# Kernel tuning notes

Hardware: AMD Instinct MI355X
Metric: run time of the kernel (lower is better)

The kernel has to match this reference:

```python
import jax, jax.numpy as jnp
import numpy as np
from jax import lax

BATCH, SEQ_LEN, HIDDEN, CLASSES = 512, 256, 1024, 128

def _xavier(key, shape):
    fan_out, fan_in = shape
    std = float(np.sqrt(2.0 / (fan_in + fan_out)))
    return jax.random.normal(key, shape, dtype=jnp.float32) * std

def setup_inputs() -> dict:
    key = jax.random.key(0)
    k_x, k_hx, k_hh, k_ph = jax.random.split(key, 4)
    return {
        "x": jax.random.normal(k_x, (BATCH, SEQ_LEN), dtype=jnp.float32),
        "W_hx": _xavier(k_hx, (HIDDEN, 1)),
        "W_hh": _xavier(k_hh, (HIDDEN, HIDDEN)),
        "b_h": jnp.zeros((HIDDEN,), dtype=jnp.float32),
        "W_ph": _xavier(k_ph, (CLASSES, HIDDEN)),
        "b_p": jnp.zeros((CLASSES,), dtype=jnp.float32),
    }

def reference(x, W_hx, W_hh, b_h, W_ph, b_p):
    # x: [B, T] (input_dim == 1 per timestep, as in the torch module)
    B = x.shape[0]
    H = W_hh.shape[0]
    h0 = jnp.zeros((B, H), dtype=x.dtype)

    def step(h, xt):
        # xt: [B]; xt[:, None] @ W_hx.T -> [B, H]
        h_new = jnp.tanh(xt[:, None] @ W_hx.T + h @ W_hh.T + b_h)
        return h_new, None

    h_last, _ = lax.scan(step, h0, x.T)  # scan over time: x.T is [T, B]
    # Output head applied to final hidden state (loop's last p in torch code)
    return h_last @ W_ph.T + b_p  # [B, num_classes]
```

## Files before the change

kernel.cpp:

```cpp
#include <hip/hip_runtime.h>
#include <stdint.h>


#define BATCH 512
#define SEQ   256
#define HID   1024
#define CLS   128

#define GB 16
#define GJ 16
#define BT 32
#define JT 64
#define KC 256
#define SSTR 260
#define HSTR 68
#define HS_OFF 16384
#define SMEM_BYTES (32768 + BT * HSTR * 2)
#define HBUF_HALVES (BATCH * HID)

typedef __attribute__((ext_vector_type(8))) short  bf16x8;
typedef __attribute__((ext_vector_type(4))) short  s16x4;
typedef __attribute__((ext_vector_type(4))) float  f32x4;
typedef __attribute__((ext_vector_type(4))) int    i32x4;
typedef __attribute__((ext_vector_type(2))) unsigned int u32x2;

__device__ __forceinline__ unsigned short f2bf(float f) {
  unsigned int u = __float_as_uint(f);
  u = (u + 0x7FFFu + ((u >> 16) & 1u)) >> 16;
  return (unsigned short)u;
}
__device__ __forceinline__ float b2f(short h) {
  return __uint_as_float(((unsigned int)(unsigned short)h) << 16);
}

__device__ __forceinline__ void store_flag(int* p, int v) {
  asm volatile("global_store_dword %0, %1, off sc0 sc1" :: "v"(p), "v"(v) : "memory");
}
__device__ __forceinline__ int load_flag(const int* p) {
  int v;
  asm volatile("global_load_dword %0, %1, off sc0 sc1\n\t"
               "s_waitcnt vmcnt(0)" : "=v"(v) : "v"(p) : "memory");
  return v;
}
__device__ __forceinline__ void store16(void* p, i32x4 v) {
  asm volatile("global_store_dwordx4 %0, %1, off sc0 sc1" :: "v"(p), "v"(v) : "memory");
}
__device__ __forceinline__ void waitcnt0() {
  asm volatile("s_waitcnt vmcnt(0)" ::: "memory");
}
__device__ __forceinline__ void barrier_lgkm() {
  asm volatile("s_waitcnt lgkmcnt(0)\n\ts_barrier" ::: "memory");
}
__device__ __forceinline__ void issue4(const void* p, i32x4& a, i32x4& b, i32x4& c, i32x4& d) {
  asm volatile(
    "global_load_dwordx4 %0, %4, off sc0 sc1\n\t"
    "global_load_dwordx4 %1, %4, off offset:128 sc0 sc1\n\t"
    "global_load_dwordx4 %2, %4, off offset:256 sc0 sc1\n\t"
    "global_load_dwordx4 %3, %4, off offset:384 sc0 sc1"
    : "=&v"(a), "=&v"(b), "=&v"(c), "=&v"(d)
    : "v"(p) : "memory");
}
__device__ __forceinline__ void issue4_64(const void* p, i32x4& a, i32x4& b, i32x4& c, i32x4& d) {
  asm volatile(
    "global_load_dwordx4 %0, %4, off sc0 sc1\n\t"
    "global_load_dwordx4 %1, %4, off offset:64 sc0 sc1\n\t"
    "global_load_dwordx4 %2, %4, off offset:128 sc0 sc1\n\t"
    "global_load_dwordx4 %3, %4, off offset:192 sc0 sc1"
    : "=&v"(a), "=&v"(b), "=&v"(c), "=&v"(d)
    : "v"(p) : "memory");
}

__device__ __forceinline__ void wr16(short* p, i32x4 v) {
  u32x2 lo, hi;
  lo.x = (unsigned)v.x; lo.y = (unsigned)v.y;
  hi.x = (unsigned)v.z; hi.y = (unsigned)v.w;
  *(u32x2*)p = lo;
  *(u32x2*)(p + 4) = hi;
}
__device__ __forceinline__ float tanh_fast(float z) {
  float e = __expf(2.f * z);
  return 1.f - 2.f / (e + 1.f);
}

#define MFMA(a, b, c) __builtin_amdgcn_mfma_f32_16x16x32_bf16((a), (b), (c), 0, 0, 0)

__global__ void __launch_bounds__(256, 1)
rnn_persistent(const float* __restrict__ x, const float* __restrict__ Whx,
               const float* __restrict__ Whh, const float* __restrict__ bh,
               const float* __restrict__ Wph, const float* __restrict__ bp,
               float* __restrict__ out, unsigned short* hbuf, int* flags)
{
  extern __shared__ short smem[];
  float* scr = (float*)smem;
  short* hS  = smem + HS_OFF;

  const int tid  = threadIdx.x;
  const int bg   = blockIdx.x & 15;
  const int jg   = blockIdx.x >> 4;
  const int lane = tid & 63;
  const int wv   = tid >> 6;
  const int l15  = lane & 15;
  const int quad = lane >> 4;

  bf16x8 barr[4][8];
#pragma unroll
  for (int ct = 0; ct < 4; ++ct) {
#pragma unroll
    for (int ks = 0; ks < 8; ++ks) {
      const float* wp = Whh + (jg * JT + ct * 16 + l15) * HID
                            + wv * 256 + ks * 32 + quad * 8;
      float4 fA = *(const float4*)(wp);
      float4 fB = *(const float4*)(wp + 4);
      union { bf16x8 v8; s16x4 h[2]; } u;
      u.h[0].x = (short)f2bf(fA.x); u.h[0].y = (short)f2bf(fA.y);
      u.h[0].z = (short)f2bf(fA.z); u.h[0].w = (short)f2bf(fA.w);
      u.h[1].x = (short)f2bf(fB.x); u.h[1].y = (short)f2bf(fB.y);
      u.h[1].z = (short)f2bf(fB.z); u.h[1].w = (short)f2bf(fB.w);
      barr[ct][ks] = u.v8;
    }
  }

  const int j = jg * JT + wv * 16 + l15;
  const float whx = Whx[j];
  const float bhv = bh[j];
  const int grow0 = bg * BT + quad * 4;

  const int sr  = tid >> 3;
  const int seg = tid & 7;

  int* myflags = flags + bg * 64;

  for (int t = 0; t < SEQ; ++t) {
    const unsigned short* hin = hbuf + ((t + 1) & 1) * HBUF_HALVES;
    unsigned short*      hout = hbuf + (t & 1) * HBUF_HALVES;

    f32x4 acc00 = {0,0,0,0}, acc01 = {0,0,0,0}, acc02 = {0,0,0,0}, acc03 = {0,0,0,0};
    f32x4 acc10 = {0,0,0,0}, acc11 = {0,0,0,0}, acc12 = {0,0,0,0}, acc13 = {0,0,0,0};

    float xv0[4], xv1[4];
    {
      const float* xp = x + grow0 * SEQ + t;
#pragma unroll
      for (int rg = 0; rg < 4; ++rg) {
        xv0[rg] = xp[rg * SEQ];
        xv1[rg] = xp[(16 + rg) * SEQ];
      }
    }

    if (t > 0) {
      if (lane < 4) {
        while (load_flag(myflags + wv * 4 + lane) < t) {
          asm volatile("s_sleep 1" ::: "memory");
        }
      }

      const short* pA0 = (const short*)hin + (bg * BT + l15) * HID
                         + wv * 256 + quad * 8;
      const short* pA1 = pA0 + 16 * HID;
      i32x4 A0, A1, A2, A3, A4, A5, A6, A7, A8, A9, A10, A11, A12, A13, A14, A15;
      issue4_64(pA0,        A0,  A1,  A2,  A3);
      issue4_64(pA0 + 128,  A4,  A5,  A6,  A7);
      issue4_64(pA1,        A8,  A9,  A10, A11);
      issue4_64(pA1 + 128,  A12, A13, A14, A15);

      asm volatile("s_waitcnt vmcnt(0)"
                   : "+v"(A0), "+v"(A1), "+v"(A2),  "+v"(A3),
                     "+v"(A4), "+v"(A5), "+v"(A6),  "+v"(A7),
                     "+v"(A8), "+v"(A9), "+v"(A10), "+v"(A11),
                     "+v"(A12), "+v"(A13), "+v"(A14), "+v"(A15)
                   :: "memory");
      __builtin_amdgcn_sched_barrier(0);

#define KSTEP(Ar0, Ar1, KS) { \
      bf16x8 _a0 = *(const bf16x8*)&(Ar0); \
      bf16x8 _a1 = *(const bf16x8*)&(Ar1); \
      acc00 = MFMA(_a0, barr[0][KS], acc00); acc10 = MFMA(_a1, barr[0][KS], acc10); \
      acc01 = MFMA(_a0, barr[1][KS], acc01); acc11 = MFMA(_a1, barr[1][KS], acc11); \
      acc02 = MFMA(_a0, barr[2][KS], acc02); acc12 = MFMA(_a1, barr[2][KS], acc12); \
      acc03 = MFMA(_a0, barr[3][KS], acc03); acc13 = MFMA(_a1, barr[3][KS], acc13); }
      KSTEP(A0, A8,  0) KSTEP(A1, A9,  1) KSTEP(A2, A10, 2) KSTEP(A3, A11, 3)
      KSTEP(A4, A12, 4) KSTEP(A5, A13, 5) KSTEP(A6, A14, 6) KSTEP(A7, A15, 7)
#undef KSTEP
    }

    barrier_lgkm();
#pragma unroll
    for (int ct = 0; ct < 4; ++ct) {
      f32x4 w0 = (ct == 0) ? acc00 : (ct == 1) ? acc01 : (ct == 2) ? acc02 : acc03;
      f32x4 w1 = (ct == 0) ? acc10 : (ct == 1) ? acc11 : (ct == 2) ? acc12 : acc13;
      *(f32x4*)(scr + (((ct * 2 + 0) * 4 + wv) * 64 + lane) * 4) = w0;
      *(f32x4*)(scr + (((ct * 2 + 1) * 4 + wv) * 64 + lane) * 4) = w1;
    }
    barrier_lgkm();
    {
      f32x4 f0 = {0,0,0,0}, f1 = {0,0,0,0};
#pragma unroll
      for (int w = 0; w < 4; ++w) {
        f0 += *(const f32x4*)(scr + (((wv * 2 + 0) * 4 + w) * 64 + lane) * 4);
        f1 += *(const f32x4*)(scr + (((wv * 2 + 1) * 4 + w) * 64 + lane) * 4);
      }
#pragma unroll
      for (int rg = 0; rg < 4; ++rg) {
        float z0 = f0[rg] + xv0[rg] * whx + bhv;
        hS[(quad * 4 + rg) * HSTR + wv * 16 + l15] = (short)f2bf(tanh_fast(z0));
        float z1 = f1[rg] + xv1[rg] * whx + bhv;
        hS[(16 + quad * 4 + rg) * HSTR + wv * 16 + l15] = (short)f2bf(tanh_fast(z1));
      }
    }
    barrier_lgkm();
    {
      const short* hsrc = hS + sr * HSTR + seg * 8;
      u32x2 lo = *(const u32x2*)(hsrc);
      u32x2 hi = *(const u32x2*)(hsrc + 4);
      i32x4 sv; sv.x = (int)lo.x; sv.y = (int)lo.y; sv.z = (int)hi.x; sv.w = (int)hi.y;
      unsigned short* dst = hout + (bg * BT + sr) * HID + jg * JT + seg * 8;
      store16(dst, sv);
    }
    waitcnt0();
    barrier_lgkm();
    if (tid == 0) store_flag(myflags + jg, t + 1);
  }

  if (tid < GJ) {
    while (load_flag(myflags + tid) < SEQ) {
      asm volatile("s_sleep 1" ::: "memory");
    }
  }
  __syncthreads();

  const unsigned short* hlast = hbuf + ((SEQ - 1) & 1) * HBUF_HALVES;
  short* sS = smem;
  const int cc = tid & 7;
  const int cg = jg * 8 + cc;
  const int hr = tid >> 3;
  float acc = 0.f;
  const char* lbase = (const char*)(hlast + (bg * BT + sr) * HID) + seg * 16;
  short* sdst = sS + sr * SSTR + seg * 8;
  for (int c = 0; c < 4; ++c) {
    __syncthreads();
    i32x4 p0, p1, p2, p3;
    issue4(lbase + c * 512, p0, p1, p2, p3);
    waitcnt0();
    wr16(sdst, p0); wr16(sdst + 64, p1); wr16(sdst + 128, p2); wr16(sdst + 192, p3);
    __syncthreads();
    const float* wp = Wph + cg * HID + c * KC;
    const short* hs = sS + hr * SSTR;
#pragma unroll 8
    for (int k4 = 0; k4 < 64; ++k4) {
      float4 w  = *(const float4*)(wp + k4 * 4);
      s16x4 hv  = *(const s16x4*)(hs + k4 * 4);
      acc += b2f(hv.x) * w.x + b2f(hv.y) * w.y + b2f(hv.z) * w.z + b2f(hv.w) * w.w;
    }
  }
  out[(bg * BT + hr) * CLS + cg] = acc + bp[cg];
}

extern "C" void kernel_launch(void* const* d_in, const int* in_sizes, int n_in,
                              void* d_out, int out_size, void* d_ws, size_t ws_size,
                              hipStream_t stream) {
  const float* x   = (const float*)d_in[0];
  const float* Whx = (const float*)d_in[1];
  const float* Whh = (const float*)d_in[2];
  const float* bh  = (const float*)d_in[3];
  const float* Wph = (const float*)d_in[4];
  const float* bp  = (const float*)d_in[5];
  float* out = (float*)d_out;

  unsigned short* hbuf = (unsigned short*)d_ws;
  int* flags = (int*)((char*)d_ws + (size_t)2 * HBUF_HALVES * 2);

  hipMemsetAsync(flags, 0, GB * 64 * sizeof(int), stream);

  hipFuncSetAttribute(reinterpret_cast<const void*>(rnn_persistent),
                      hipFuncAttributeMaxDynamicSharedMemorySize, SMEM_BYTES);

  rnn_persistent<<<dim3(GB * GJ), dim3(256), SMEM_BYTES, stream>>>(
      x, Whx, Whh, bh, Wph, bp, out, hbuf, flags);
}
```

Baseline: 1.156 ms.

## Repartition persistent RNN grid into 32 batch groups by 8 hidden groups

Reshapes the persistent grid from 16x16 tiles (32 batch rows x 64 hidden columns) to 32x8 tiles (16 batch rows x 128 hidden columns). Each block now keeps twice as many W_hh register fragments and loads half as much h per step. Each batch group waits on 8 producer flags instead of 16, and a block-wide sync is added after the flag poll. The output-head epilogue stages the whole final hidden row into shared memory at once instead of in four chunks. This cuts per-step cross-block synchronisation fan-in and h traffic, at the cost of higher register pressure, which could cause spills.

Measured after the change: 966.0 us, median of 2. 16.4% less time.

```diff
diff --git a/kernel.cpp b/kernel.cpp
--- a/kernel.cpp
+++ b/kernel.cpp
@@ -7,13 +7,11 @@
 #define HID   1024
 #define CLS   128
 
-#define GB 16
-#define GJ 16
-#define BT 32
-#define JT 64
-#define KC 256
-#define SSTR 260
-#define HSTR 68
+#define GB 32
+#define GJ 8
+#define BT 16
+#define JT 128
+#define HSTR 132
 #define HS_OFF 16384
 #define SMEM_BYTES (32768 + BT * HSTR * 2)
 #define HBUF_HALVES (BATCH * HID)
@@ -50,15 +48,6 @@
 }
 __device__ __forceinline__ void barrier_lgkm() {
   asm volatile("s_waitcnt lgkmcnt(0)\n\ts_barrier" ::: "memory");
-}
-__device__ __forceinline__ void issue4(const void* p, i32x4& a, i32x4& b, i32x4& c, i32x4& d) {
-  asm volatile(
-    "global_load_dwordx4 %0, %4, off sc0 sc1\n\t"
-    "global_load_dwordx4 %1, %4, off offset:128 sc0 sc1\n\t"
-    "global_load_dwordx4 %2, %4, off offset:256 sc0 sc1\n\t"
-    "global_load_dwordx4 %3, %4, off offset:384 sc0 sc1"
-    : "=&v"(a), "=&v"(b), "=&v"(c), "=&v"(d)
-    : "v"(p) : "memory");
 }
 __device__ __forceinline__ void issue4_64(const void* p, i32x4& a, i32x4& b, i32x4& c, i32x4& d) {
   asm volatile(
@@ -66,6 +55,15 @@
     "global_load_dwordx4 %1, %4, off offset:64 sc0 sc1\n\t"
     "global_load_dwordx4 %2, %4, off offset:128 sc0 sc1\n\t"
     "global_load_dwordx4 %3, %4, off offset:192 sc0 sc1"
+    : "=&v"(a), "=&v"(b), "=&v"(c), "=&v"(d)
+    : "v"(p) : "memory");
+}
+__device__ __forceinline__ void issue4_16(const void* p, i32x4& a, i32x4& b, i32x4& c, i32x4& d) {
+  asm volatile(
+    "global_load_dwordx4 %0, %4, off sc0 sc1\n\t"
+    "global_load_dwordx4 %1, %4, off offset:16 sc0 sc1\n\t"
+    "global_load_dwordx4 %2, %4, off offset:32 sc0 sc1\n\t"
+    "global_load_dwordx4 %3, %4, off offset:48 sc0 sc1"
     : "=&v"(a), "=&v"(b), "=&v"(c), "=&v"(d)
     : "v"(p) : "memory");
 }
@@ -95,16 +93,16 @@
   short* hS  = smem + HS_OFF;
 
   const int tid  = threadIdx.x;
-  const int bg   = blockIdx.x & 15;
-  const int jg   = blockIdx.x >> 4;
+  const int bg   = blockIdx.x & 31;
+  const int jg   = blockIdx.x >> 5;
   const int lane = tid & 63;
   const int wv   = tid >> 6;
   const int l15  = lane & 15;
   const int quad = lane >> 4;
 
-  bf16x8 barr[4][8];
-#pragma unroll
-  for (int ct = 0; ct < 4; ++ct) {
+  bf16x8 barr[8][8];
+#pragma unroll
+  for (int ct = 0; ct < 8; ++ct) {
 #pragma unroll
     for (int ks = 0; ks < 8; ++ks) {
       const float* wp = Whh + (jg * JT + ct * 16 + l15) * HID
@@ -120,13 +118,13 @@
     }
   }
 
-  const int j = jg * JT + wv * 16 + l15;
-  const float whx = Whx[j];
-  const float bhv = bh[j];
-  const int grow0 = bg * BT + quad * 4;
-
-  const int sr  = tid >> 3;
-  const int seg = tid & 7;
+  const int j0 = jg * JT + wv * 32 + l15;
+  const int j1 = j0 + 16;
+  const float whx0 = Whx[j0], whx1 = Whx[j1];
+  const float bhv0 = bh[j0],  bhv1 = bh[j1];
+
+  const int sr  = tid >> 4;
+  const int seg = tid & 15;
 
   int* myflags = flags + bg * 64;
 
@@ -134,77 +132,69 @@
     const unsigned short* hin = hbuf + ((t + 1) & 1) * HBUF_HALVES;
     unsigned short*      hout = hbuf + (t & 1) * HBUF_HALVES;
 
-    f32x4 acc00 = {0,0,0,0}, acc01 = {0,0,0,0}, acc02 = {0,0,0,0}, acc03 = {0,0,0,0};
-    f32x4 acc10 = {0,0,0,0}, acc11 = {0,0,0,0}, acc12 = {0,0,0,0}, acc13 = {0,0,0,0};
-
-    float xv0[4], xv1[4];
+    f32x4 acc0 = {0,0,0,0}, acc1 = {0,0,0,0}, acc2 = {0,0,0,0}, acc3 = {0,0,0,0};
+    f32x4 acc4 = {0,0,0,0}, acc5 = {0,0,0,0}, acc6 = {0,0,0,0}, acc7 = {0,0,0,0};
+
+    float xv[4];
     {
-      const float* xp = x + grow0 * SEQ + t;
-#pragma unroll
-      for (int rg = 0; rg < 4; ++rg) {
-        xv0[rg] = xp[rg * SEQ];
-        xv1[rg] = xp[(16 + rg) * SEQ];
-      }
+      const float* xp = x + (bg * BT + quad * 4) * SEQ + t;
+#pragma unroll
+      for (int rg = 0; rg < 4; ++rg) xv[rg] = xp[rg * SEQ];
     }
 
     if (t > 0) {
-      if (lane < 4) {
-        while (load_flag(myflags + wv * 4 + lane) < t) {
+      if (tid < GJ) {
+        while (load_flag(myflags + tid) < t) {
           asm volatile("s_sleep 1" ::: "memory");
         }
       }
-
-      const short* pA0 = (const short*)hin + (bg * BT + l15) * HID
-                         + wv * 256 + quad * 8;
-      const short* pA1 = pA0 + 16 * HID;
-      i32x4 A0, A1, A2, A3, A4, A5, A6, A7, A8, A9, A10, A11, A12, A13, A14, A15;
-      issue4_64(pA0,        A0,  A1,  A2,  A3);
-      issue4_64(pA0 + 128,  A4,  A5,  A6,  A7);
-      issue4_64(pA1,        A8,  A9,  A10, A11);
-      issue4_64(pA1 + 128,  A12, A13, A14, A15);
+      __syncthreads();
+
+      const short* pA = (const short*)hin + (bg * BT + l15) * HID
+                        + wv * 256 + quad * 8;
+      i32x4 A0, A1, A2, A3, A4, A5, A6, A7;
+      issue4_64(pA,       A0, A1, A2, A3);
+      issue4_64(pA + 128, A4, A5, A6, A7);
 
       asm volatile("s_waitcnt vmcnt(0)"
-                   : "+v"(A0), "+v"(A1), "+v"(A2),  "+v"(A3),
-                     "+v"(A4), "+v"(A5), "+v"(A6),  "+v"(A7),
-                     "+v"(A8), "+v"(A9), "+v"(A10), "+v"(A11),
-                     "+v"(A12), "+v"(A13), "+v"(A14), "+v"(A15)
+                   : "+v"(A0), "+v"(A1), "+v"(A2), "+v"(A3),
+                     "+v"(A4), "+v"(A5), "+v"(A6), "+v"(A7)
                    :: "memory");
       __builtin_amdgcn_sched_barrier(0);
 
-#define KSTEP(Ar0, Ar1, KS) { \
-      bf16x8 _a0 = *(const bf16x8*)&(Ar0); \
-      bf16x8 _a1 = *(const bf16x8*)&(Ar1); \
-      acc00 = MFMA(_a0, barr[0][KS], acc00); acc10 = MFMA(_a1, barr[0][KS], acc10); \
-      acc01 = MFMA(_a0, barr[1][KS], acc01); acc11 = MFMA(_a1, barr[1][KS], acc11); \
-      acc02 = MFMA(_a0, barr[2][KS], acc02); acc12 = MFMA(_a1, barr[2][KS], acc12); \
-      acc03 = MFMA(_a0, barr[3][KS], acc03); acc13 = MFMA(_a1, barr[3][KS], acc13); }
-      KSTEP(A0, A8,  0) KSTEP(A1, A9,  1) KSTEP(A2, A10, 2) KSTEP(A3, A11, 3)
-      KSTEP(A4, A12, 4) KSTEP(A5, A13, 5) KSTEP(A6, A14, 6) KSTEP(A7, A15, 7)
+#define KSTEP(Ar, KS) { \
+      bf16x8 _a = *(const bf16x8*)&(Ar); \
+      acc0 = MFMA(_a, barr[0][KS], acc0); acc1 = MFMA(_a, barr[1][KS], acc1); \
+      acc2 = MFMA(_a, barr[2][KS], acc2); acc3 = MFMA(_a, barr[3][KS], acc3); \
+      acc4 = MFMA(_a, barr[4][KS], acc4); acc5 = MFMA(_a, barr[5][KS], acc5); \
+      acc6 = MFMA(_a, barr[6][KS], acc6); acc7 = MFMA(_a, barr[7][KS], acc7); }
+      KSTEP(A0, 0) KSTEP(A1, 1) KSTEP(A2, 2) KSTEP(A3, 3)
+      KSTEP(A4, 4) KSTEP(A5, 5) KSTEP(A6, 6) KSTEP(A7, 7)
 #undef KSTEP
     }
 
     barrier_lgkm();
 #pragma unroll
-    for (int ct = 0; ct < 4; ++ct) {
-      f32x4 w0 = (ct == 0) ? acc00 : (ct == 1) ? acc01 : (ct == 2) ? acc02 : acc03;
-      f32x4 w1 = (ct == 0) ? acc10 : (ct == 1) ? acc11 : (ct == 2) ? acc12 : acc13;
-      *(f32x4*)(scr + (((ct * 2 + 0) * 4 + wv) * 64 + lane) * 4) = w0;
-      *(f32x4*)(scr + (((ct * 2 + 1) * 4 + wv) * 64 + lane) * 4) = w1;
+    for (int ct = 0; ct < 8; ++ct) {
+      f32x4 w = (ct == 0) ? acc0 : (ct == 1) ? acc1 : (ct == 2) ? acc2 :
+                (ct == 3) ? acc3 : (ct == 4) ? acc4 : (ct == 5) ? acc5 :
+                (ct == 6) ? acc6 : acc7;
+      *(f32x4*)(scr + ((ct * 4 + wv) * 64 + lane) * 4) = w;
     }
     barrier_lgkm();
     {
       f32x4 f0 = {0,0,0,0}, f1 = {0,0,0,0};
 #pragma unroll
       for (int w = 0; w < 4; ++w) {
-        f0 += *(const f32x4*)(scr + (((wv * 2 + 0) * 4 + w) * 64 + lane) * 4);
-        f1 += *(const f32x4*)(scr + (((wv * 2 + 1) * 4 + w) * 64 + lane) * 4);
+        f0 += *(const f32x4*)(scr + (((2 * wv)     * 4 + w) * 64 + lane) * 4);
+        f1 += *(const f32x4*)(scr + (((2 * wv + 1) * 4 + w) * 64 + lane) * 4);
       }
 #pragma unroll
       for (int rg = 0; rg < 4; ++rg) {
-        float z0 = f0[rg] + xv0[rg] * whx + bhv;
-        hS[(quad * 4 + rg) * HSTR + wv * 16 + l15] = (short)f2bf(tanh_fast(z0));
-        float z1 = f1[rg] + xv1[rg] * whx + bhv;
-        hS[(16 + quad * 4 + rg) * HSTR + wv * 16 + l15] = (short)f2bf(tanh_fast(z1));
+        float z0 = f0[rg] + xv[rg] * whx0 + bhv0;
+        hS[(quad * 4 + rg) * HSTR + wv * 32 + l15] = (short)f2bf(tanh_fast(z0));
+        float z1 = f1[rg] + xv[rg] * whx1 + bhv1;
+        hS[(quad * 4 + rg) * HSTR + wv * 32 + 16 + l15] = (short)f2bf(tanh_fast(z1));
       }
     }
     barrier_lgkm();
@@ -229,30 +219,32 @@
   __syncthreads();
 
   const unsigned short* hlast = hbuf + ((SEQ - 1) & 1) * HBUF_HALVES;
-  short* sS = smem;
-  const int cc = tid & 7;
-  const int cg = jg * 8 + cc;
-  const int hr = tid >> 3;
-  float acc = 0.f;
-  const char* lbase = (const char*)(hlast + (bg * BT + sr) * HID) + seg * 16;
-  short* sdst = sS + sr * SSTR + seg * 8;
-  for (int c = 0; c < 4; ++c) {
-    __syncthreads();
-    i32x4 p0, p1, p2, p3;
-    issue4(lbase + c * 512, p0, p1, p2, p3);
+  {
+    const char* lbase = (const char*)(hlast + (bg * BT + sr) * HID) + seg * 128;
+    i32x4 p0, p1, p2, p3, p4, p5, p6, p7;
+    issue4_16(lbase,      p0, p1, p2, p3);
+    issue4_16(lbase + 64, p4, p5, p6, p7);
     waitcnt0();
-    wr16(sdst, p0); wr16(sdst + 64, p1); wr16(sdst + 128, p2); wr16(sdst + 192, p3);
-    __syncthreads();
-    const float* wp = Wph + cg * HID + c * KC;
-    const short* hs = sS + hr * SSTR;
+    short* sdst = smem + sr * 1028 + seg * 64;
+    wr16(sdst,      p0); wr16(sdst + 8,  p1); wr16(sdst + 16, p2); wr16(sdst + 24, p3);
+    wr16(sdst + 32, p4); wr16(sdst + 40, p5); wr16(sdst + 48, p6); wr16(sdst + 56, p7);
+  }
+  __syncthreads();
+  {
+    const int hr = tid >> 4;
+    const int cc = tid & 15;
+    const int cg = jg * 16 + cc;
+    const float* wp = Wph + cg * HID;
+    const short* hs = smem + hr * 1028;
+    float acc = 0.f;
 #pragma unroll 8
-    for (int k4 = 0; k4 < 64; ++k4) {
+    for (int k4 = 0; k4 < 256; ++k4) {
       float4 w  = *(const float4*)(wp + k4 * 4);
       s16x4 hv  = *(const s16x4*)(hs + k4 * 4);
       acc += b2f(hv.x) * w.x + b2f(hv.y) * w.y + b2f(hv.z) * w.z + b2f(hv.w) * w.w;
     }
-  }
-  out[(bg * BT + hr) * CLS + cg] = acc + bp[cg];
+    out[(bg * BT + hr) * CLS + cg] = acc + bp[cg];
+  }
 }
 
 extern "C" void kernel_launch(void* const* d_in, const int* in_sizes, int n_in,
```
